# Kernel optimization log

Hardware: AMD Instinct MI355X
Metric: run time of the kernel (lower is better)

## Reference

```python
import jax, jax.numpy as jnp
import numpy as np

B, T, D, H = 2, 2048, 1024, 16
DH = D // H  # head dim = 64


def setup_inputs() -> dict:
    key = jax.random.key(0)
    ks = jax.random.split(key, 10)
    s = D ** -0.5
    inp = {
        "x": jax.random.normal(ks[0], (B, T, D), jnp.float32),
        "data_mask": jax.random.randint(ks[1], (B, T), 0, 2, jnp.int32),
        "Wq": jax.random.normal(ks[2], (D, D), jnp.float32) * s,
        "bq": jnp.zeros((D,), jnp.float32),
        "Wk": jax.random.normal(ks[3], (D, D), jnp.float32) * s,
        "bk": jnp.zeros((D,), jnp.float32),
        "Wv": jax.random.normal(ks[4], (D, D), jnp.float32) * s,
        "bv": jnp.zeros((D,), jnp.float32),
        "Wp": jax.random.normal(ks[5], (D, D), jnp.float32) * s,
        "bp": jnp.zeros((D,), jnp.float32),
    }
    return inp


def _split_heads(t):
    # [B, T, D] -> [B, H, T, DH]
    return jnp.swapaxes(t.reshape(B, T, H, DH), 1, 2)


def reference(x, data_mask, Wq, bq, Wk, bk, Wv, bv, Wp, bp):
    q = _split_heads(x @ Wq + bq)
    k = _split_heads(x @ Wk + bk)  # kv = x (self-attention)
    v = _split_heads(x @ Wv + bv)

    # combined mask: causal tri AND data_mask outer product -> [B, 1, T, T]
    dm = data_mask.astype(bool)
    causal = jnp.tril(jnp.ones((T, T), bool))
    mask = causal[None, None] & (dm[:, None, :, None] & dm[:, None, None, :])

    q = q * (DH ** -0.5)  # scale_logits
    scores = jnp.einsum('bhqd,bhkd->bhqk', q, k)  # [B, H, T, T]
    scores = jnp.where(mask, scores, -jnp.inf)
    weights = jax.nn.softmax(scores, axis=-1)
    weights = jnp.nan_to_num(weights)  # fully-masked rows -> 0
    o = jnp.einsum('bhqk,bhkd->bhqd', weights, v)

    # recover shape: [B, H, T, DH] -> [B, T, D]
    o = jnp.swapaxes(o, 1, 2).reshape(B, T, D)
    o = o @ Wp + bp

    # linear mask: multiply output by data_mask [B, T, 1]
    o = o * data_mask.astype(o.dtype)[..., None]
    return o
```

## Files before the change

kernel.cpp:

```cpp
#include <hip/hip_runtime.h>
#include <hip/hip_bf16.h>
#include <cstdint>
#include <cstddef>

#define Bb 2
#define Tt 2048
#define Dd 1024
#define Hh 16
#define DHh 64

using short8 = __attribute__((ext_vector_type(8))) short;
using f32x4  = __attribute__((ext_vector_type(4))) float;
typedef unsigned short u16;

__device__ __forceinline__ u16 f2bf(float f) {
    unsigned int u = __float_as_uint(f);
    u += 0x7fffu + ((u >> 16) & 1u);
    return (u16)(u >> 16);
}

__device__ __forceinline__ unsigned int pk2bf(float a, float b) {
    union { __hip_bfloat162 h; unsigned int u; } c;
    c.h = __float22bfloat162_rn(float2{a, b});
    return c.u;
}

__device__ __forceinline__ void gload16(const void* g, void* l) {
    __builtin_amdgcn_global_load_lds((const __attribute__((address_space(1))) void*)g,
                                     (__attribute__((address_space(3))) void*)l, 16, 0, 0);
}

__device__ __forceinline__ void gemm_bt_core(const u16* __restrict__ A, const u16* __restrict__ BT,
                                             int K, int m0, int n0,
                                             u16* As, u16* Bs, f32x4 acc[4][4]) {
    const int tid = threadIdx.x;
    const int w = tid >> 6, lane = tid & 63;
    const int lr = lane & 15, lg = lane >> 4;
    const int wr = w >> 1, wc = w & 1;
    const int arow = lane >> 2;
    const int acol = (lane & 3) * 8;
    for (int kk = 0; kk < K; kk += 32) {
        __syncthreads();
#pragma unroll
        for (int j = 0; j < 2; ++j) {
            int r0 = w * 32 + j * 16;
            gload16(A  + (size_t)(m0 + r0 + arow) * K + kk + acol, (char*)As + r0 * 64);
            gload16(BT + (size_t)(n0 + r0 + arow) * K + kk + acol, (char*)Bs + r0 * 64);
        }
        __syncthreads();
        short8 af[4], bfv[4];
#pragma unroll
        for (int m = 0; m < 4; ++m)
            af[m] = *(const short8*)((const char*)As + ((wr * 64 + m * 16 + lr) * 64 + lg * 16));
#pragma unroll
        for (int n = 0; n < 4; ++n)
            bfv[n] = *(const short8*)((const char*)Bs + ((wc * 64 + n * 16 + lr) * 64 + lg * 16));
#pragma unroll
        for (int m = 0; m < 4; ++m)
#pragma unroll
            for (int n = 0; n < 4; ++n)
                acc[m][n] = __builtin_amdgcn_mfma_f32_16x16x32_bf16(af[m], bfv[n], acc[m][n], 0, 0, 0);
    }
}

__global__ __launch_bounds__(256) void convert_x_k(const float4* __restrict__ x4,
                                                   ushort4* __restrict__ xb4, int n4,
                                                   const int* __restrict__ dmask,
                                                   float* __restrict__ dmf) {
    int i = blockIdx.x * 256 + threadIdx.x;
    if (i < n4) {
        float4 v = x4[i];
        ushort4 o;
        o.x = f2bf(v.x); o.y = f2bf(v.y); o.z = f2bf(v.z); o.w = f2bf(v.w);
        xb4[i] = o;
    }
    if (i < Bb * Tt) dmf[i] = (float)dmask[i];
}

__global__ void transpose_w_k(const float* __restrict__ Wq, const float* __restrict__ Wk,
                              const float* __restrict__ Wv, const float* __restrict__ Wp,
                              u16* __restrict__ wt) {
    __shared__ float tile[32][33];
    const int z = blockIdx.z;
    const float* W = (z == 0) ? Wq : (z == 1) ? Wk : (z == 2) ? Wv : Wp;
    const int n0 = blockIdx.x * 32, k0 = blockIdx.y * 32;
    const int tx = threadIdx.x, ty = threadIdx.y;
#pragma unroll
    for (int j = 0; j < 4; ++j)
        tile[ty + j * 8][tx] = W[(size_t)(k0 + ty + j * 8) * Dd + n0 + tx];
    __syncthreads();
    u16* outp = wt + (size_t)z * Dd * Dd;
#pragma unroll
    for (int j = 0; j < 4; ++j)
        outp[(size_t)(n0 + ty + j * 8) * Dd + k0 + tx] = f2bf(tile[tx][ty + j * 8]);
}

__global__ __launch_bounds__(256) void qkv_gemm_k(const u16* __restrict__ xb, const u16* __restrict__ wt,
        const float* __restrict__ bq, const float* __restrict__ bk, const float* __restrict__ bv,
        u16* __restrict__ Qg, u16* __restrict__ Kg, u16* __restrict__ VTg) {
    __shared__ alignas(16) u16 As[128 * 32];
    __shared__ alignas(16) u16 Bs[128 * 32];
    f32x4 acc[4][4];
    const f32x4 vzero = {0.f, 0.f, 0.f, 0.f};
#pragma unroll
    for (int m = 0; m < 4; ++m)
#pragma unroll
        for (int n = 0; n < 4; ++n) acc[m][n] = vzero;
    const int m0 = blockIdx.y * 128, n0 = blockIdx.x * 128;
    gemm_bt_core(xb, wt, 1024, m0, n0, As, Bs, acc);
    const int tid = threadIdx.x, w = tid >> 6, lane = tid & 63, lr = lane & 15, lg = lane >> 4;
    const int wr = w >> 1, wc = w & 1;
    const int sec = n0 >> 10;
    const float* bias = (sec == 0) ? bq : (sec == 1) ? bk : bv;
    u16* dst = (sec == 0) ? Qg : (sec == 1) ? Kg : VTg;
    const float qscale = (sec == 0) ? 0.125f * 1.4426950408889634f : 1.0f;
#pragma unroll
    for (int n = 0; n < 4; ++n) {
        int gn = n0 + wc * 64 + n * 16 + lr;
        int j = gn & 1023;
        float bj = bias[j];
        int h = j >> 6, dh = j & 63;
#pragma unroll
        for (int m = 0; m < 4; ++m) {
            int gmb = m0 + wr * 64 + m * 16 + 4 * lg;
#pragma unroll
            for (int i = 0; i < 4; ++i) {
                int gm = gmb + i;
                int b = gm >> 11, t = gm & 2047;
                float v = (acc[m][n][i] + bj) * qscale;
                size_t off;
                if (sec < 2) off = (((size_t)(b * Hh + h)) * Tt + t) * DHh + dh;
                else         off = (((size_t)(b * Hh + h)) * DHh + dh) * Tt + t;
                dst[off] = f2bf(v);
            }
        }
    }
}

__global__ __launch_bounds__(256) void attn_k(const u16* __restrict__ Qg, const u16* __restrict__ Kg,
        const u16* __restrict__ VTg, const float* __restrict__ dmf, u16* __restrict__ Og) {
    __shared__ alignas(16) u16 Ks[128 * 64];
    __shared__ alignas(16) u16 Vs[64 * 128];
    __shared__ alignas(16) u16 Ps[4][16 * 128];
    const int bh = blockIdx.x;
    const int qb = (int)gridDim.y - 1 - (int)blockIdx.y;
    const int b = bh >> 4, h = bh & 15;
    const int tid = threadIdx.x, w = tid >> 6, lane = tid & 63;
    const int lr = lane & 15, lg = lane >> 4;
    const int q0 = qb * 64 + w * 16;
    const int qrow = q0 + lr;
    const u16* Qbase = Qg + ((size_t)bh * Tt + q0) * DHh;
    short8 qf0 = *(const short8*)(Qbase + lr * DHh + lg * 8);
    short8 qf1 = *(const short8*)(Qbase + lr * DHh + 32 + lg * 8);
    const f32x4 vzero = {0.f, 0.f, 0.f, 0.f};
    const short8 ones8 = {(short)0x3F80, (short)0x3F80, (short)0x3F80, (short)0x3F80,
                          (short)0x3F80, (short)0x3F80, (short)0x3F80, (short)0x3F80};
    f32x4 o[4];
#pragma unroll
    for (int n = 0; n < 4; ++n) o[n] = vzero;
    f32x4 acc_l = vzero;
    const int ktiles = (qb * 64 + 63) / 128 + 1;
    char* KsB = (char*)Ks; char* VsB = (char*)Vs; char* PsB = (char*)&Ps[w][0];

    for (int kt = 0; kt < ktiles; ++kt) {
        const int kbase = kt * 128;
        __syncthreads();
#pragma unroll
        for (int j = 0; j < 4; ++j) {
            int r0 = w * 32 + j * 8;
            int r = r0 + (lane >> 3);
            int cs = (lane & 7) ^ (r & 7);
            gload16(Kg + ((size_t)bh * Tt + kbase + r) * DHh + cs * 8, KsB + r0 * 128);
        }
#pragma unroll
        for (int j = 0; j < 4; ++j) {
            int r0 = w * 16 + j * 4;
            int r = r0 + (lane >> 4);
            int cs = (lane & 15) ^ (r & 7);
            gload16(VTg + ((size_t)bh * DHh + r) * Tt + kbase + cs * 8, VsB + r0 * 256);
        }
        __syncthreads();
        f32x4 s[8];
#pragma unroll
        for (int nf = 0; nf < 8; ++nf) {
            int r = nf * 16 + lr;
            short8 k0v = *(const short8*)(KsB + r * 128 + (((0 + lg) ^ (r & 7)) << 4));
            short8 k1v = *(const short8*)(KsB + r * 128 + (((4 + lg) ^ (r & 7)) << 4));
            f32x4 t0 = __builtin_amdgcn_mfma_f32_16x16x32_bf16(k0v, qf0, vzero, 0, 0, 0);
            s[nf] = __builtin_amdgcn_mfma_f32_16x16x32_bf16(k1v, qf1, t0, 0, 0, 0);
        }
        float4 km[8];
        {
            const float4* dmv = (const float4*)(dmf + (size_t)b * Tt + kbase);
#pragma unroll
            for (int nf = 0; nf < 8; ++nf) km[nf] = dmv[4 * nf + lg];
        }
        if (kbase + 127 > q0) {
#pragma unroll
            for (int nf = 0; nf < 8; ++nf) {
                int tk = kbase + 16 * nf + 4 * lg;
                if (tk + 0 > qrow) km[nf].x = 0.f;
                if (tk + 1 > qrow) km[nf].y = 0.f;
                if (tk + 2 > qrow) km[nf].z = 0.f;
                if (tk + 3 > qrow) km[nf].w = 0.f;
            }
        }
#pragma unroll
        for (int nf = 0; nf < 8; ++nf) {
            float p0 = exp2f(s[nf][0]) * km[nf].x;
            float p1 = exp2f(s[nf][1]) * km[nf].y;
            float p2 = exp2f(s[nf][2]) * km[nf].z;
            float p3 = exp2f(s[nf][3]) * km[nf].w;
            uint2 pw;
            pw.x = pk2bf(p0, p1);
            pw.y = pk2bf(p2, p3);
            *(uint2*)(PsB + lr * 256 + ((((2 * nf + (lg >> 1)) ^ (lr & 7))) << 4) + ((lg & 1) << 3)) = pw;
        }
#pragma unroll
        for (int ks = 0; ks < 4; ++ks) {
            short8 pf = *(const short8*)(PsB + lr * 256 + ((((ks * 4 + lg)) ^ (lr & 7)) << 4));
            acc_l = __builtin_amdgcn_mfma_f32_16x16x32_bf16(ones8, pf, acc_l, 0, 0, 0);
#pragma unroll
            for (int n = 0; n < 4; ++n) {
                int rv = n * 16 + lr;
                short8 vf = *(const short8*)(VsB + rv * 256 + ((((ks * 4 + lg)) ^ (rv & 7)) << 4));
                o[n] = __builtin_amdgcn_mfma_f32_16x16x32_bf16(vf, pf, o[n], 0, 0, 0);
            }
        }
    }
    float l = acc_l[0];
    float inv = l > 0.f ? 1.0f / l : 0.f;
#pragma unroll
    for (int n = 0; n < 4; ++n) {
        uint2 pw;
        pw.x = pk2bf(o[n][0] * inv, o[n][1] * inv);
        pw.y = pk2bf(o[n][2] * inv, o[n][3] * inv);
        *(uint2*)(Og + ((size_t)(b * Tt + qrow)) * Dd + h * DHh + n * 16 + 4 * lg) = pw;
    }
}

__global__ __launch_bounds__(256) void out_gemm_k(const u16* __restrict__ Og, const u16* __restrict__ wpt,
        const float* __restrict__ bp, const int* __restrict__ dmask, float* __restrict__ out) {
    __shared__ alignas(16) u16 As[128 * 32];
    __shared__ alignas(16) u16 Bs[128 * 32];
    f32x4 acc[4][4];
    const f32x4 vzero = {0.f, 0.f, 0.f, 0.f};
#pragma unroll
    for (int m = 0; m < 4; ++m)
#pragma unroll
        for (int n = 0; n < 4; ++n) acc[m][n] = vzero;
    const int m0 = blockIdx.y * 128, n0 = blockIdx.x * 128;
    gemm_bt_core(Og, wpt, 1024, m0, n0, As, Bs, acc);
    const int tid = threadIdx.x, w = tid >> 6, lane = tid & 63, lr = lane & 15, lg = lane >> 4;
    const int wr = w >> 1, wc = w & 1;
#pragma unroll
    for (int n = 0; n < 4; ++n) {
        int gn = n0 + wc * 64 + n * 16 + lr;
        float bj = bp[gn];
#pragma unroll
        for (int m = 0; m < 4; ++m) {
            int gmb = m0 + wr * 64 + m * 16 + 4 * lg;
#pragma unroll
            for (int i = 0; i < 4; ++i) {
                int gm = gmb + i;
                float dmv = (float)dmask[gm];
                out[(size_t)gm * Dd + gn] = (acc[m][n][i] + bj) * dmv;
            }
        }
    }
}

extern "C" void kernel_launch(void* const* d_in, const int* in_sizes, int n_in,
                              void* d_out, int out_size, void* d_ws, size_t ws_size,
                              hipStream_t stream) {
    const float* x   = (const float*)d_in[0];
    const int*  dmask = (const int*)d_in[1];
    const float* Wq = (const float*)d_in[2];
    const float* bq = (const float*)d_in[3];
    const float* Wk = (const float*)d_in[4];
    const float* bk = (const float*)d_in[5];
    const float* Wv = (const float*)d_in[6];
    const float* bv = (const float*)d_in[7];
    const float* Wp = (const float*)d_in[8];
    const float* bp = (const float*)d_in[9];
    float* out = (float*)d_out;
    char* ws = (char*)d_ws;
    u16* xb  = (u16*)(ws);
    u16* wt  = (u16*)(ws + ((size_t)8 << 20));
    u16* Qg  = (u16*)(ws + ((size_t)16 << 20));
    u16* Kg  = (u16*)(ws + ((size_t)24 << 20));
    u16* VTg = (u16*)(ws + ((size_t)32 << 20));
    float* dmf = (float*)(ws + ((size_t)40 << 20));
    u16* Og  = xb;

    convert_x_k<<<dim3(4096), dim3(256), 0, stream>>>((const float4*)x, (ushort4*)xb,
                                                      (Bb * Tt * Dd) / 4, dmask, dmf);
    transpose_w_k<<<dim3(32, 32, 4), dim3(32, 8), 0, stream>>>(Wq, Wk, Wv, Wp, wt);
    qkv_gemm_k<<<dim3(24, 32), dim3(256), 0, stream>>>(xb, wt, bq, bk, bv, Qg, Kg, VTg);
    attn_k<<<dim3(32, 32), dim3(256), 0, stream>>>(Qg, Kg, VTg, dmf, Og);
    out_gemm_k<<<dim3(8, 32), dim3(256), 0, stream>>>(Og, wt + (size_t)3 * Dd * Dd, bp, dmask, out);
}
```

Baseline: 126.0 us.

## Keep attention probabilities in registers, fold mask into MFMA bias, pre-tile V

The data mask becomes an additive bias (0 or -15000). It is fed as the accumulator input to the QK MFMA, and the causal mask subtracts the same constant. This removes the multiply-by-mask step. The P tile no longer round-trips through shared memory: V^T is written by the QKV GEMM in a permuted, pre-swizzled tiled layout, so the MFMA register layout of exp(S) can be used directly as the B operand and V loads become contiguous. Launch bounds request 4 blocks per CU, and the additive bias relies on exp2(-15000) underflowing to zero in place of exact masking.

```diff
diff --git a/kernel.cpp b/kernel.cpp
--- a/kernel.cpp
+++ b/kernel.cpp
@@ -66,7 +66,7 @@
 __global__ __launch_bounds__(256) void convert_x_k(const float4* __restrict__ x4,
                                                    ushort4* __restrict__ xb4, int n4,
                                                    const int* __restrict__ dmask,
-                                                   float* __restrict__ dmf) {
+                                                   float* __restrict__ dmb) {
     int i = blockIdx.x * 256 + threadIdx.x;
     if (i < n4) {
         float4 v = x4[i];
@@ -74,7 +74,7 @@
         o.x = f2bf(v.x); o.y = f2bf(v.y); o.z = f2bf(v.z); o.w = f2bf(v.w);
         xb4[i] = o;
     }
-    if (i < Bb * Tt) dmf[i] = (float)dmask[i];
+    if (i < Bb * Tt) dmb[i] = dmask[i] ? 0.f : -15000.f;
 }
 
 __global__ void transpose_w_k(const float* __restrict__ Wq, const float* __restrict__ Wk,
@@ -130,18 +130,23 @@
                 float v = (acc[m][n][i] + bj) * qscale;
                 size_t off;
                 if (sec < 2) off = (((size_t)(b * Hh + h)) * Tt + t) * DHh + dh;
-                else         off = (((size_t)(b * Hh + h)) * DHh + dh) * Tt + t;
+                else {
+                    int kt2 = t >> 7, a = t & 127;
+                    int ks2 = a >> 5, r = a & 31;
+                    int pos = ks2 * 32 + ((r & 15) >> 2) * 8 + ((r >> 4) & 1) * 4 + (r & 3);
+                    int chunkp = (pos >> 3) ^ (dh & 7);
+                    off = (((size_t)(b * Hh + h) * 16 + kt2) * 64 + dh) * 128 + chunkp * 8 + (pos & 7);
+                }
                 dst[off] = f2bf(v);
             }
         }
     }
 }
 
-__global__ __launch_bounds__(256) void attn_k(const u16* __restrict__ Qg, const u16* __restrict__ Kg,
-        const u16* __restrict__ VTg, const float* __restrict__ dmf, u16* __restrict__ Og) {
+__global__ __launch_bounds__(256, 4) void attn_k(const u16* __restrict__ Qg, const u16* __restrict__ Kg,
+        const u16* __restrict__ VTg, const float* __restrict__ dmb, u16* __restrict__ Og) {
     __shared__ alignas(16) u16 Ks[128 * 64];
     __shared__ alignas(16) u16 Vs[64 * 128];
-    __shared__ alignas(16) u16 Ps[4][16 * 128];
     const int bh = blockIdx.x;
     const int qb = (int)gridDim.y - 1 - (int)blockIdx.y;
     const int b = bh >> 4, h = bh & 15;
@@ -160,7 +165,7 @@
     for (int n = 0; n < 4; ++n) o[n] = vzero;
     f32x4 acc_l = vzero;
     const int ktiles = (qb * 64 + 63) / 128 + 1;
-    char* KsB = (char*)Ks; char* VsB = (char*)Vs; char* PsB = (char*)&Ps[w][0];
+    char* KsB = (char*)Ks; char* VsB = (char*)Vs;
 
     for (int kt = 0; kt < ktiles; ++kt) {
         const int kbase = kt * 128;
@@ -172,59 +177,46 @@
             int cs = (lane & 7) ^ (r & 7);
             gload16(Kg + ((size_t)bh * Tt + kbase + r) * DHh + cs * 8, KsB + r0 * 128);
         }
-#pragma unroll
-        for (int j = 0; j < 4; ++j) {
-            int r0 = w * 16 + j * 4;
-            int r = r0 + (lane >> 4);
-            int cs = (lane & 15) ^ (r & 7);
-            gload16(VTg + ((size_t)bh * DHh + r) * Tt + kbase + cs * 8, VsB + r0 * 256);
+        {
+            const u16* vsrc = VTg + (((size_t)bh * 16 + kt) * 8192) + w * 2048 + lane * 8;
+#pragma unroll
+            for (int j = 0; j < 4; ++j)
+                gload16(vsrc + j * 512, VsB + w * 4096 + j * 1024);
         }
         __syncthreads();
         f32x4 s[8];
+        const float* bb = dmb + (size_t)b * Tt + kbase + 4 * lg;
 #pragma unroll
         for (int nf = 0; nf < 8; ++nf) {
             int r = nf * 16 + lr;
             short8 k0v = *(const short8*)(KsB + r * 128 + (((0 + lg) ^ (r & 7)) << 4));
             short8 k1v = *(const short8*)(KsB + r * 128 + (((4 + lg) ^ (r & 7)) << 4));
-            f32x4 t0 = __builtin_amdgcn_mfma_f32_16x16x32_bf16(k0v, qf0, vzero, 0, 0, 0);
+            f32x4 cin = *(const f32x4*)(bb + nf * 16);
+            f32x4 t0 = __builtin_amdgcn_mfma_f32_16x16x32_bf16(k0v, qf0, cin, 0, 0, 0);
             s[nf] = __builtin_amdgcn_mfma_f32_16x16x32_bf16(k1v, qf1, t0, 0, 0, 0);
-        }
-        float4 km[8];
-        {
-            const float4* dmv = (const float4*)(dmf + (size_t)b * Tt + kbase);
-#pragma unroll
-            for (int nf = 0; nf < 8; ++nf) km[nf] = dmv[4 * nf + lg];
         }
         if (kbase + 127 > q0) {
 #pragma unroll
             for (int nf = 0; nf < 8; ++nf) {
                 int tk = kbase + 16 * nf + 4 * lg;
-                if (tk + 0 > qrow) km[nf].x = 0.f;
-                if (tk + 1 > qrow) km[nf].y = 0.f;
-                if (tk + 2 > qrow) km[nf].z = 0.f;
-                if (tk + 3 > qrow) km[nf].w = 0.f;
-            }
-        }
-#pragma unroll
-        for (int nf = 0; nf < 8; ++nf) {
-            float p0 = exp2f(s[nf][0]) * km[nf].x;
-            float p1 = exp2f(s[nf][1]) * km[nf].y;
-            float p2 = exp2f(s[nf][2]) * km[nf].z;
-            float p3 = exp2f(s[nf][3]) * km[nf].w;
-            uint2 pw;
-            pw.x = pk2bf(p0, p1);
-            pw.y = pk2bf(p2, p3);
-            *(uint2*)(PsB + lr * 256 + ((((2 * nf + (lg >> 1)) ^ (lr & 7))) << 4) + ((lg & 1) << 3)) = pw;
+#pragma unroll
+                for (int i = 0; i < 4; ++i)
+                    if (tk + i > qrow) s[nf][i] -= 15000.f;
+            }
         }
 #pragma unroll
         for (int ks = 0; ks < 4; ++ks) {
-            short8 pf = *(const short8*)(PsB + lr * 256 + ((((ks * 4 + lg)) ^ (lr & 7)) << 4));
-            acc_l = __builtin_amdgcn_mfma_f32_16x16x32_bf16(ones8, pf, acc_l, 0, 0, 0);
+            union { uint4 u; short8 sv; } pf;
+            pf.u.x = pk2bf(exp2f(s[2 * ks][0]), exp2f(s[2 * ks][1]));
+            pf.u.y = pk2bf(exp2f(s[2 * ks][2]), exp2f(s[2 * ks][3]));
+            pf.u.z = pk2bf(exp2f(s[2 * ks + 1][0]), exp2f(s[2 * ks + 1][1]));
+            pf.u.w = pk2bf(exp2f(s[2 * ks + 1][2]), exp2f(s[2 * ks + 1][3]));
+            acc_l = __builtin_amdgcn_mfma_f32_16x16x32_bf16(ones8, pf.sv, acc_l, 0, 0, 0);
 #pragma unroll
             for (int n = 0; n < 4; ++n) {
                 int rv = n * 16 + lr;
                 short8 vf = *(const short8*)(VsB + rv * 256 + ((((ks * 4 + lg)) ^ (rv & 7)) << 4));
-                o[n] = __builtin_amdgcn_mfma_f32_16x16x32_bf16(vf, pf, o[n], 0, 0, 0);
+                o[n] = __builtin_amdgcn_mfma_f32_16x16x32_bf16(vf, pf.sv, o[n], 0, 0, 0);
             }
         }
     }
@@ -290,13 +282,13 @@
     u16* Qg  = (u16*)(ws + ((size_t)16 << 20));
     u16* Kg  = (u16*)(ws + ((size_t)24 << 20));
     u16* VTg = (u16*)(ws + ((size_t)32 << 20));
-    float* dmf = (float*)(ws + ((size_t)40 << 20));
+    float* dmb = (float*)(ws + ((size_t)40 << 20));
     u16* Og  = xb;
 
     convert_x_k<<<dim3(4096), dim3(256), 0, stream>>>((const float4*)x, (ushort4*)xb,
-                                                      (Bb * Tt * Dd) / 4, dmask, dmf);
+                                                      (Bb * Tt * Dd) / 4, dmask, dmb);
     transpose_w_k<<<dim3(32, 32, 4), dim3(32, 8), 0, stream>>>(Wq, Wk, Wv, Wp, wt);
     qkv_gemm_k<<<dim3(24, 32), dim3(256), 0, stream>>>(xb, wt, bq, bk, bv, Qg, Kg, VTg);
-    attn_k<<<dim3(32, 32), dim3(256), 0, stream>>>(Qg, Kg, VTg, dmf, Og);
+    attn_k<<<dim3(32, 32), dim3(256), 0, stream>>>(Qg, Kg, VTg, dmb, Og);
     out_gemm_k<<<dim3(8, 32), dim3(256), 0, stream>>>(Og, wt + (size_t)3 * Dd * Dd, bp, dmask, out);
 }
```

Measured after the change: 113.7 us. 1.11x faster.
